# Performance work log

Hardware: AMD Instinct MI355X
Metric: run time of the kernel (lower is better)

## Reference

```python
import jax, jax.numpy as jnp
import numpy as np

HID = 2048          # hidden_size
INTER = 4096        # expand * hidden_size
NH = 64             # num_heads
HD = 64             # head_dim (NH*HD == INTER)
N = 128             # ssm state_size
G = 1               # n_groups
K = 4               # conv_kernel
EPS = 1e-5
CONV_DIM = INTER + 2 * G * N            # 4352
PROJ = INTER + CONV_DIM + NH            # 8512 (d_mlp == 0)


def setup_inputs() -> dict:
    key = jax.random.key(0)
    ks = jax.random.split(key, 6)
    B, S = 2, 2048
    return {
        "hidden_states": jax.random.normal(ks[0], (B, S, HID), jnp.float32),
        "in_proj_w": jax.random.normal(ks[1], (PROJ, HID), jnp.float32) * 0.02,
        "conv_w": jax.random.normal(ks[2], (CONV_DIM, 1, K), jnp.float32) * 0.1,
        "conv_b": jax.random.normal(ks[3], (CONV_DIM,), jnp.float32) * 0.02,
        "dt_bias": jnp.ones((NH,), jnp.float32),
        "A_log": jnp.log(jnp.arange(1, NH + 1, dtype=jnp.float32)),
        "D": jnp.ones((NH,), jnp.float32),
        "norm_weight": jnp.ones((INTER,), jnp.float32),
        "out_proj_w": jax.random.normal(ks[4], (HID, INTER), jnp.float32) * 0.02,
    }


def _mamba2_forward(hidden_states, in_proj_w, conv_w, conv_b, dt_bias,
                    A_log, D, norm_weight, out_proj_w):
    b, sq, _ = hidden_states.shape
    # in_proj (d_mlp == 0, so split is gate | hidden_B_C | dt)
    proj = hidden_states @ in_proj_w.T                       # [b, s, PROJ]
    gate, hbc, dt = jnp.split(proj, [INTER, INTER + CONV_DIM], axis=-1)

    # causal depthwise conv1d over time + SiLU
    xc = jnp.transpose(hbc, (0, 2, 1))                       # [b, conv_dim, s]
    xc = jax.lax.conv_general_dilated(xc, conv_w, (1,), [(K - 1, 0)],
                                      feature_group_count=CONV_DIM)
    xc = xc + conv_b[None, :, None]
    hbc = jax.nn.silu(jnp.transpose(xc, (0, 2, 1)))          # [b, s, conv_dim]

    hs, Bm, Cm = jnp.split(hbc, [INTER, INTER + G * N], axis=-1)
    hs = hs.reshape(b, sq, NH, HD)
    Bm = jnp.repeat(Bm.reshape(b, sq, G, N), NH // G, axis=2)   # [b, s, nh, n]
    Cm = jnp.repeat(Cm.reshape(b, sq, G, N), NH // G, axis=2)

    A = -jnp.exp(A_log)                                      # [nh]
    dt = jax.nn.softplus(dt + dt_bias)                       # [b, s, nh]

    # selective SSM scan: state_t = exp(dt*A)*state_{t-1} + dt*B_t x_t^T
    def step(state, inp):
        xt, Bt, Ct, dtt = inp                                # [b,nh,hd],[b,nh,n],[b,nh,n],[b,nh]
        dA = jnp.exp(dtt * A)                                # [b, nh]
        state = state * dA[..., None, None] \
            + (dtt[..., None] * xt)[..., None] * Bt[:, :, None, :]
        y = jnp.einsum('bhdn,bhn->bhd', state, Ct)
        return state, y

    init = jnp.zeros((b, NH, HD, N), jnp.float32)
    xs = (jnp.moveaxis(hs, 1, 0), jnp.moveaxis(Bm, 1, 0),
          jnp.moveaxis(Cm, 1, 0), jnp.moveaxis(dt, 1, 0))
    _, ys = jax.lax.scan(step, init, xs)                     # [s, b, nh, hd]
    y = jnp.moveaxis(ys, 0, 1) + D[None, None, :, None] * hs
    y = y.reshape(b, sq, INTER)

    # gated RMSNorm (norm_before_gate=False): gate first, then normalize
    y = y * jax.nn.silu(gate)
    var = jnp.mean(y * y, axis=-1, keepdims=True)
    y = y * jax.lax.rsqrt(var + EPS) * norm_weight
    return y @ out_proj_w.T                                  # [b, s, HID]


def reference(hidden_states, in_proj_w, conv_w, conv_b, dt_bias, A_log, D,
              norm_weight, out_proj_w):
    return _mamba2_forward(hidden_states, in_proj_w, conv_w, conv_b, dt_bias,
                           A_log, D, norm_weight, out_proj_w)
```

## Files before the change

kernel.cpp:

```cpp
#include <hip/hip_runtime.h>
#include <hip/hip_bf16.h>
#include <cstddef>
#include <cstdint>

#define HID   2048
#define INTER 4096
#define NH    64
#define HD    64
#define NST   128
#define CONV_DIM 4352
#define PROJ  8512
#define PROJ_PAD 8704
#define SS    2048
#define BB    2
#define BS    (BB*SS)
#define EPS   1e-5f

#define COL_HS 4096
#define COL_B  8192
#define COL_C  8320
#define COL_DT 8448

#define NCH   16
#define CHUNK 128

#define CL    128
#define NCHK  16

typedef short s16x8 __attribute__((ext_vector_type(8)));
typedef float f32x4 __attribute__((ext_vector_type(4)));

__device__ inline ushort f2b(float x) {
  __hip_bfloat16 h = __float2bfloat16(x);
  return *(ushort*)&h;
}
__device__ inline float b2f(ushort u) {
  unsigned int v = ((unsigned int)u) << 16;
  return __uint_as_float(v);
}
__device__ inline int swz(int row, int e) { return row * 128 + (e ^ ((row & 7) << 3)); }

__device__ inline void gload16(const void* g, void* l) {
  __builtin_amdgcn_global_load_lds((const __attribute__((address_space(1))) void*)g,
                                   (__attribute__((address_space(3))) void*)l, 16, 0, 0);
}

__global__ __launch_bounds__(256) void to_bf16(const float* __restrict__ src,
                                               ushort* __restrict__ dst, long n4) {
  long i = (long)blockIdx.x * 256 + threadIdx.x;
  if (i >= n4) return;
  float4 v = *(const float4*)(src + i * 4);
  ushort4 o;
  o.x = f2b(v.x); o.y = f2b(v.y); o.z = f2b(v.z); o.w = f2b(v.w);
  *(ushort4*)(dst + i * 4) = o;
}

__global__ __launch_bounds__(256) void to_bf16_pad(const float* __restrict__ src,
                                                   ushort* __restrict__ dst, long n4) {
  long i = (long)blockIdx.x * 256 + threadIdx.x;
  if (i >= n4) return;
  long e0 = i * 4;
  long row = e0 >> 11;
  ushort4 o;
  if (row < PROJ) {
    float4 v = *(const float4*)(src + e0);
    o.x = f2b(v.x); o.y = f2b(v.y); o.z = f2b(v.z); o.w = f2b(v.w);
  } else {
    o.x = o.y = o.z = o.w = 0;
  }
  *(ushort4*)(dst + e0) = o;
}

__global__ __launch_bounds__(512, 2) void gemm256_8ph(
    const ushort* __restrict__ A, const ushort* __restrict__ Bw,
    ushort* __restrict__ C, float* __restrict__ dtbuf) {
  __shared__ ushort smem[65536];
  const int tid = threadIdx.x;
  const int lane = tid & 63;
  const int wid = tid >> 6;
  const int wm = wid >> 2;
  const int wn = wid & 3;
  const int r = lane & 15;
  const int kx = lane >> 4;

  const int fid = blockIdx.x;
  const int bcol = ((fid >> 7) << 3) + ((fid & 127) >> 4);
  const int brow = fid & 15;

  const ushort* Ag = A + (size_t)(brow * 256) * HID;
  const ushort* Bg = Bw + (size_t)(bcol * 256) * HID;

  const int srow = tid >> 3;
  const int scole = (((tid & 7) * 16) ^ ((srow & 7) << 4)) >> 1;

  auto stageA = [&](int buf, int kt, int half) {
    const ushort* g = Ag + (size_t)(half * 128 + srow) * HID + kt * 64 + scole;
    ushort* l = smem + buf * 16384 + half * 8192 + tid * 8;
    gload16(g, l);
    gload16(g + (size_t)64 * HID, l + 4096);
  };
  auto stageB = [&](int buf, int kt, int half) {
    const ushort* g = Bg + (size_t)(half * 128 + srow) * HID + kt * 64 + scole;
    ushort* l = smem + 32768 + buf * 16384 + half * 8192 + tid * 8;
    gload16(g, l);
    gload16(g + (size_t)64 * HID, l + 4096);
  };
  auto ldA = [&](int buf, int mf, int ks) -> s16x8 {
    int row = wm * 128 + mf * 16 + r;
    int cb = (ks * 64 + kx * 16) ^ ((row & 7) << 4);
    return *(const s16x8*)(smem + buf * 16384 + row * 64 + (cb >> 1));
  };
  auto ldB = [&](int buf, int nf, int ks) -> s16x8 {
    int row = wn * 64 + nf * 16 + r;
    int cb = (ks * 64 + kx * 16) ^ ((row & 7) << 4);
    return *(const s16x8*)(smem + 32768 + buf * 16384 + row * 64 + (cb >> 1));
  };

  f32x4 acc[8][4];
#pragma unroll
  for (int i = 0; i < 8; i++)
#pragma unroll
    for (int j = 0; j < 4; j++) acc[i][j] = (f32x4)0.f;

  constexpr int NT = HID / 64;

  stageA(0, 0, 0); stageA(0, 0, 1);
  stageB(0, 0, 0); stageB(0, 0, 1);
  stageA(1, 1, 0); stageA(1, 1, 1);
  stageB(1, 1, 0); stageB(1, 1, 1);
  asm volatile("s_waitcnt vmcnt(8)" ::: "memory");
  __builtin_amdgcn_s_barrier();

  int cur = 0;
  for (int t = 0; t < NT; t++) {
    s16x8 a[4][2], b[2][2], b2[2][2];
#pragma unroll
    for (int mf = 0; mf < 4; mf++)
#pragma unroll
      for (int ks = 0; ks < 2; ks++) a[mf][ks] = ldA(cur, mf, ks);
#pragma unroll
    for (int nf = 0; nf < 2; nf++)
#pragma unroll
      for (int ks = 0; ks < 2; ks++) b[nf][ks] = ldB(cur, nf, ks);
    __builtin_amdgcn_s_barrier();
    asm volatile("s_waitcnt lgkmcnt(0)" ::: "memory");
    __builtin_amdgcn_sched_barrier(0);
    __builtin_amdgcn_s_setprio(1);
#pragma unroll
    for (int mf = 0; mf < 4; mf++)
#pragma unroll
      for (int nf = 0; nf < 2; nf++)
#pragma unroll
        for (int ks = 0; ks < 2; ks++)
          acc[mf][nf] = __builtin_amdgcn_mfma_f32_16x16x32_bf16(a[mf][ks], b[nf][ks], acc[mf][nf], 0, 0, 0);
    __builtin_amdgcn_s_setprio(0);
    __builtin_amdgcn_s_barrier();
#pragma unroll
    for (int nf = 0; nf < 2; nf++)
#pragma unroll
      for (int ks = 0; ks < 2; ks++) b2[nf][ks] = ldB(cur, nf + 2, ks);
    __builtin_amdgcn_s_barrier();
    asm volatile("s_waitcnt lgkmcnt(0)" ::: "memory");
    __builtin_amdgcn_sched_barrier(0);
    __builtin_amdgcn_s_setprio(1);
#pragma unroll
    for (int mf = 0; mf < 4; mf++)
#pragma unroll
      for (int nf = 0; nf < 2; nf++)
#pragma unroll
        for (int ks = 0; ks < 2; ks++)
          acc[mf][nf + 2] = __builtin_amdgcn_mfma_f32_16x16x32_bf16(a[mf][ks], b2[nf][ks], acc[mf][nf + 2], 0, 0, 0);
    __builtin_amdgcn_s_setprio(0);
    __builtin_amdgcn_s_barrier();
#pragma unroll
    for (int mf = 0; mf < 4; mf++)
#pragma unroll
      for (int ks = 0; ks < 2; ks++) a[mf][ks] = ldA(cur, mf + 4, ks);
    __builtin_amdgcn_s_barrier();
    asm volatile("s_waitcnt lgkmcnt(0)" ::: "memory");
    __builtin_amdgcn_sched_barrier(0);
    __builtin_amdgcn_s_setprio(1);
#pragma unroll
    for (int mf = 0; mf < 4; mf++)
#pragma unroll
      for (int nf = 0; nf < 2; nf++)
#pragma unroll
        for (int ks = 0; ks < 2; ks++)
          acc[mf + 4][nf] = __builtin_amdgcn_mfma_f32_16x16x32_bf16(a[mf][ks], b[nf][ks], acc[mf + 4][nf], 0, 0, 0);
    __builtin_amdgcn_s_setprio(0);
    __builtin_amdgcn_s_barrier();
    if (t + 2 < NT) {
      stageA(cur, t + 2, 0); stageA(cur, t + 2, 1);
      stageB(cur, t + 2, 0); stageB(cur, t + 2, 1);
    }
    __builtin_amdgcn_s_setprio(1);
#pragma unroll
    for (int mf = 0; mf < 4; mf++)
#pragma unroll
      for (int nf = 0; nf < 2; nf++)
#pragma unroll
        for (int ks = 0; ks < 2; ks++)
          acc[mf + 4][nf + 2] = __builtin_amdgcn_mfma_f32_16x16x32_bf16(a[mf][ks], b2[nf][ks], acc[mf + 4][nf + 2], 0, 0, 0);
    __builtin_amdgcn_s_setprio(0);
    if (t + 2 < NT) {
      asm volatile("s_waitcnt vmcnt(8)" ::: "memory");
    } else {
      asm volatile("s_waitcnt vmcnt(0)" ::: "memory");
    }
    __builtin_amdgcn_s_barrier();
    cur ^= 1;
  }

  const int m0 = brow * 256 + wm * 128 + (lane >> 4) * 4;
  const int n0 = bcol * 256 + wn * 64 + r;
#pragma unroll
  for (int mf = 0; mf < 8; mf++) {
#pragma unroll
    for (int nf = 0; nf < 4; nf++) {
      int n = n0 + nf * 16;
      if (n >= PROJ) continue;
#pragma unroll
      for (int q = 0; q < 4; q++) {
        float v = acc[mf][nf][q];
        int m = m0 + mf * 16 + q;
        C[(size_t)m * PROJ + n] = f2b(v);
        if (n >= COL_DT) dtbuf[(size_t)m * 64 + (n - COL_DT)] = v;
      }
    }
  }
}

__global__ __launch_bounds__(256) void gemm_bt16(
    const ushort* __restrict__ A, int lda,
    const ushort* __restrict__ Bw, int ldb,
    float* __restrict__ C, int ldc, int Kd) {
  __shared__ short smem[8192];
  const int tid = threadIdx.x;
  const int lane = tid & 63;
  const int wid = tid >> 6;
  const int wm = wid >> 1, wn = wid & 1;
  const int r = lane & 15;
  const int kx = lane >> 4;

  const int fid = blockIdx.y * gridDim.x + blockIdx.x;
  const int bcol = ((fid >> 8) << 3) | ((fid & 255) >> 5);
  const int brow = fid & 31;

  const ushort* Ab = A + (size_t)(brow * 128) * lda;
  const ushort* Bb = Bw + (size_t)(bcol * 128) * ldb;

  f32x4 acc[4][4];
#pragma unroll
  for (int i = 0; i < 4; i++)
#pragma unroll
    for (int j = 0; j < 4; j++) acc[i][j] = (f32x4)0.f;

  const int u0 = tid, u1 = 256 + tid;
  const int row0 = u0 >> 2, kc0 = (u0 & 3) * 8;
  const int row1 = u1 >> 2, kc1 = (u1 & 3) * 8;

  const s16x8* As8 = (const s16x8*)smem;
  const s16x8* Bs8 = (const s16x8*)(smem + 4096);

  for (int k0 = 0; k0 < Kd; k0 += 32) {
    __syncthreads();
    gload16(Ab + (size_t)row0 * lda + k0 + kc0, smem + u0 * 8);
    gload16(Ab + (size_t)row1 * lda + k0 + kc1, smem + u1 * 8);
    gload16(Bb + (size_t)row0 * ldb + k0 + kc0, smem + 4096 + u0 * 8);
    gload16(Bb + (size_t)row1 * ldb + k0 + kc1, smem + 4096 + u1 * 8);
    __syncthreads();
    s16x8 af[4], bw[4];
#pragma unroll
    for (int i = 0; i < 4; i++) af[i] = As8[(wm * 64 + i * 16 + r) * 4 + kx];
#pragma unroll
    for (int j = 0; j < 4; j++) bw[j] = Bs8[(wn * 64 + j * 16 + r) * 4 + kx];
#pragma unroll
    for (int i = 0; i < 4; i++)
#pragma unroll
      for (int j = 0; j < 4; j++)
        acc[i][j] = __builtin_amdgcn_mfma_f32_16x16x32_bf16(af[i], bw[j], acc[i][j], 0, 0, 0);
  }

  const int m0 = brow * 128 + wm * 64 + (lane >> 4) * 4;
  const int n0 = bcol * 128 + wn * 64 + (lane & 15);
#pragma unroll
  for (int i = 0; i < 4; i++) {
#pragma unroll
    for (int j = 0; j < 4; j++) {
      int n = n0 + j * 16;
#pragma unroll
      for (int q = 0; q < 4; q++) {
        C[(size_t)(m0 + i * 16 + q) * ldc + n] = acc[i][j][q];
      }
    }
  }
}

__global__ void conv_capture(const ushort* __restrict__ proj, ushort* __restrict__ side) {
  int idx = blockIdx.x * 256 + threadIdx.x;
  const int total = BB * CONV_DIM * NCH * 3;
  if (idx >= total) return;
  int c = idx % CONV_DIM;
  int t = idx / CONV_DIM;
  int j = t % 3; t /= 3;
  int chunk = t % NCH;
  int b = t / NCH;
  int s = chunk * CHUNK - 1 - j;
  ushort v = (s >= 0) ? proj[((size_t)b * SS + s) * PROJ + COL_HS + c] : (ushort)0;
  side[((size_t)(b * NCH + chunk) * 3 + j) * CONV_DIM + c] = v;
}

__global__ void conv_silu(ushort* __restrict__ proj, const ushort* __restrict__ side,
                          const float* __restrict__ cw, const float* __restrict__ cb) {
  int idx = blockIdx.x * 256 + threadIdx.x;
  const int total = BB * CONV_DIM * NCH;
  if (idx >= total) return;
  int c = idx % CONV_DIM;
  int t = idx / CONV_DIM;
  int chunk = t % NCH;
  int b = t / NCH;
  float w0 = cw[c * 4 + 0], w1 = cw[c * 4 + 1], w2 = cw[c * 4 + 2], w3 = cw[c * 4 + 3];
  float bias = cb[c];
  const ushort* sd = side + ((size_t)(b * NCH + chunk) * 3) * CONV_DIM;
  float xm1 = b2f(sd[c]);
  float xm2 = b2f(sd[CONV_DIM + c]);
  float xm3 = b2f(sd[2 * CONV_DIM + c]);
  size_t p = ((size_t)b * SS + (size_t)chunk * CHUNK) * PROJ + COL_HS + c;
  for (int s = 0; s < CHUNK; s++) {
    float xin = b2f(proj[p]);
    float o = w3 * xin + w2 * xm1 + w1 * xm2 + w0 * xm3 + bias;
    o = o / (1.f + __expf(-o));
    proj[p] = f2b(o);
    xm3 = xm2; xm2 = xm1; xm1 = xin;
    p += PROJ;
  }
}

__global__ __launch_bounds__(256) void ssd_chunk_state(
    const ushort* __restrict__ proj, const float* __restrict__ dtf,
    const float* __restrict__ dt_bias, const float* __restrict__ A_log,
    ushort* __restrict__ states, float* __restrict__ cumbuf,
    float* __restrict__ dtvbuf) {
  const int bid = blockIdx.x;
  const int c = bid & 15;
  const int h = (bid >> 4) & 63;
  const int b = bid >> 10;
  const int tid = threadIdx.x;
  const int lane = tid & 63;
  const int wv = tid >> 6;
  __shared__ float sdtv[CL], scum[CL], sw[CL];
  __shared__ ushort sBt[128 * 128];
  __shared__ ushort sXw[64 * 128];
  const size_t row0 = (size_t)b * SS + (size_t)c * CL;
  const size_t bh = (size_t)(b * NH + h);

  const float Ah = -__expf(A_log[h]);
  if (tid < CL) {
    float z = dtf[(row0 + tid) * 64 + h] + dt_bias[h];
    float dtv = (z > 20.f) ? z : log1pf(__expf(z));
    sdtv[tid] = dtv;
    sw[tid] = dtv * Ah;
  }
  __syncthreads();
  for (int off = 1; off < CL; off <<= 1) {
    float v = 0.f;
    if (tid < CL) { v = sw[tid]; if (tid >= off) v += sw[tid - off]; }
    __syncthreads();
    if (tid < CL) sw[tid] = v;
    __syncthreads();
  }
  if (tid < CL) {
    scum[tid] = sw[tid];
    cumbuf[bh * SS + c * CL + tid] = sw[tid];
    dtvbuf[bh * SS + c * CL + tid] = sdtv[tid];
  }
  __syncthreads();
  const float cumL = scum[CL - 1];
  if (tid < CL) sw[tid] = __expf(cumL - scum[tid]) * sdtv[tid];
  __syncthreads();

  {
    const int t = tid >> 1, n0 = (tid & 1) * 64;
    const ushort* src = proj + (row0 + t) * PROJ + COL_B + n0;
#pragma unroll
    for (int j = 0; j < 64; j += 8) {
      s16x8 v = *(const s16x8*)(src + j);
#pragma unroll
      for (int e = 0; e < 8; e++) sBt[swz(n0 + j + e, t)] = (ushort)v[e];
    }
  }
  {
    const int d = tid & 63;
    const int t0 = (tid >> 6) * 32;
    for (int t = t0; t < t0 + 32; t++) {
      float x = b2f(proj[(row0 + t) * PROJ + COL_HS + h * 64 + d]);
      sXw[swz(d, t)] = f2b(x * sw[t]);
    }
  }
  __syncthreads();

  const int r = lane & 15, kx = lane >> 4;
  f32x4 acc[2][4];
#pragma unroll
  for (int i = 0; i < 2; i++)
#pragma unroll
    for (int j = 0; j < 4; j++) acc[i][j] = (f32x4)0.f;
#pragma unroll
  for (int kk = 0; kk < 4; kk++) {
    s16x8 a[2], bo[4];
#pragma unroll
    for (int i = 0; i < 2; i++)
      a[i] = *(const s16x8*)&sBt[swz(wv * 32 + i * 16 + r, kk * 32 + kx * 8)];
#pragma unroll
    for (int j = 0; j < 4; j++)
      bo[j] = *(const s16x8*)&sXw[swz(j * 16 + r, kk * 32 + kx * 8)];
#pragma unroll
    for (int i = 0; i < 2; i++)
#pragma unroll
      for (int j = 0; j < 4; j++)
        acc[i][j] = __builtin_amdgcn_mfma_f32_16x16x32_bf16(a[i], bo[j], acc[i][j], 0, 0, 0);
  }
  ushort* dst = states + (size_t)bid * (128 * 64);
#pragma unroll
  for (int i = 0; i < 2; i++) {
#pragma unroll
    for (int j = 0; j < 4; j++) {
      int n = wv * 32 + i * 16 + (lane >> 4) * 4;
      int d = (lane & 15) + j * 16;
      ushort4 o;
      o.x = f2b(acc[i][j][0]);
      o.y = f2b(acc[i][j][1]);
      o.z = f2b(acc[i][j][2]);
      o.w = f2b(acc[i][j][3]);
      *(ushort4*)(dst + (size_t)d * 128 + n) = o;
    }
  }
}

__global__ __launch_bounds__(256) void ssd_state_scan(
    ushort* __restrict__ states, const float* __restrict__ cumbuf) {
  const int bh = blockIdx.x;
  const int tid = threadIdx.x;
  float run[32];
#pragma unroll
  for (int i = 0; i < 32; i++) run[i] = 0.f;
  for (int c = 0; c < NCHK; c++) {
    float dec = __expf(cumbuf[(size_t)bh * SS + c * CL + (CL - 1)]);
    ushort* p = states + ((size_t)bh * NCHK + c) * 8192 + tid * 32;
    s16x8 in[4];
#pragma unroll
    for (int v = 0; v < 4; v++) in[v] = *(const s16x8*)(p + v * 8);
    s16x8 out[4];
#pragma unroll
    for (int v = 0; v < 4; v++) {
#pragma unroll
      for (int e = 0; e < 8; e++) {
        int i = v * 8 + e;
        out[v][e] = (short)f2b(run[i]);
        run[i] = dec * run[i] + b2f((ushort)in[v][e]);
      }
    }
#pragma unroll
    for (int v = 0; v < 4; v++) *(s16x8*)(p + v * 8) = out[v];
  }
}

__global__ __launch_bounds__(256, 2) void ssd_chunk_out(
    ushort* __restrict__ proj, const ushort* __restrict__ states,
    const float* __restrict__ cumbuf, const float* __restrict__ dtvbuf,
    const float* __restrict__ Dp) {
  const int bid = blockIdx.x;
  const int c = bid & 15;
  const int h = (bid >> 4) & 63;
  const int b = bid >> 10;
  const int tid = threadIdx.x;
  const int lane = tid & 63;
  const int wv = tid >> 6;
  __shared__ ushort sC[128 * 128];
  __shared__ ushort sB[128 * 128];
  __shared__ ushort sX[64 * 128];
  const size_t row0 = (size_t)b * SS + (size_t)c * CL;
  const size_t bh = (size_t)(b * NH + h);
  const float* cumb = cumbuf + bh * SS + c * CL;
  const float* dtvb = dtvbuf + bh * SS + c * CL;
  const int r = lane & 15, kx = lane >> 4;

  float ct[2][4];
#pragma unroll
  for (int i = 0; i < 2; i++)
#pragma unroll
    for (int q = 0; q < 4; q++)
      ct[i][q] = cumb[wv * 32 + i * 16 + ((lane >> 4) << 2) + q];
  float cumt[8], dvt[8];
#pragma unroll
  for (int j = 0; j < 8; j++) {
    int tau = j * 16 + (lane & 15);
    cumt[j] = cumb[tau];
    dvt[j] = dtvb[tau];
  }
  const float eC = __expf(cumb[wv * 32 + (lane >> 1)]);

  {
    const int t = tid >> 1, n0 = (tid & 1) * 64;
    const ushort* srcC = proj + (row0 + t) * PROJ + COL_C + n0;
    const ushort* srcB = proj + (row0 + t) * PROJ + COL_B + n0;
#pragma unroll
    for (int j = 0; j < 64; j += 8) {
      *(s16x8*)&sC[swz(t, n0 + j)] = *(const s16x8*)(srcC + j);
      *(s16x8*)&sB[swz(t, n0 + j)] = *(const s16x8*)(srcB + j);
    }
  }
  {
    const int d = tid & 63;
    const int t0 = (tid >> 6) * 32;
    for (int t = t0; t < t0 + 32; t++)
      sX[swz(d, t)] = proj[(row0 + t) * PROJ + COL_HS + h * 64 + d];
  }
  __syncthreads();

  f32x4 g[2][8];
#pragma unroll
  for (int i = 0; i < 2; i++)
#pragma unroll
    for (int j = 0; j < 8; j++) g[i][j] = (f32x4)0.f;
#pragma unroll
  for (int kk = 0; kk < 4; kk++) {
    s16x8 a[2], bo[8];
#pragma unroll
    for (int i = 0; i < 2; i++)
      a[i] = *(const s16x8*)&sC[swz(wv * 32 + i * 16 + r, kk * 32 + kx * 8)];
#pragma unroll
    for (int j = 0; j < 8; j++)
      bo[j] = *(const s16x8*)&sB[swz(j * 16 + r, kk * 32 + kx * 8)];
#pragma unroll
    for (int i = 0; i < 2; i++)
#pragma unroll
      for (int j = 0; j < 8; j++)
        g[i][j] = __builtin_amdgcn_mfma_f32_16x16x32_bf16(a[i], bo[j], g[i][j], 0, 0, 0);
  }

  s16x8 spf[4][4];
  {
    const ushort* sp = states + (size_t)bid * 8192;
#pragma unroll
    for (int kk = 0; kk < 4; kk++)
#pragma unroll
      for (int j = 0; j < 4; j++)
        spf[kk][j] = *(const s16x8*)(sp + (size_t)(j * 16 + r) * 128 + kk * 32 + kx * 8);
  }
  __syncthreads();

#pragma unroll
  for (int j = 0; j < 8; j++) {
    float cu = cumt[j], dv = dvt[j];
    int tau = j * 16 + (lane & 15);
#pragma unroll
    for (int i = 0; i < 2; i++) {
#pragma unroll
      for (int q = 0; q < 4; q++) {
        int t = wv * 32 + i * 16 + ((lane >> 4) << 2) + q;
        float val = (tau <= t) ? g[i][j][q] * __expf(ct[i][q] - cu) * dv : 0.f;
        sB[swz(t, tau)] = f2b(val);
      }
    }
  }
  {
    int t = wv * 32 + (lane >> 1);
    int n0 = (lane & 1) * 64;
#pragma unroll
    for (int j = 0; j < 64; j += 8) {
      s16x8 u = *(const s16x8*)&sC[swz(t, n0 + j)];
#pragma unroll
      for (int k = 0; k < 8; k++) u[k] = (short)f2b(b2f((ushort)u[k]) * eC);
      *(s16x8*)&sC[swz(t, n0 + j)] = u;
    }
  }
  __syncthreads();

  f32x4 y[2][4];
#pragma unroll
  for (int i = 0; i < 2; i++)
#pragma unroll
    for (int j = 0; j < 4; j++) y[i][j] = (f32x4)0.f;
#pragma unroll
  for (int kk = 0; kk < 4; kk++) {
    s16x8 a[2], bo[4];
#pragma unroll
    for (int i = 0; i < 2; i++)
      a[i] = *(const s16x8*)&sB[swz(wv * 32 + i * 16 + r, kk * 32 + kx * 8)];
#pragma unroll
    for (int j = 0; j < 4; j++)
      bo[j] = *(const s16x8*)&sX[swz(j * 16 + r, kk * 32 + kx * 8)];
#pragma unroll
    for (int i = 0; i < 2; i++)
#pragma unroll
      for (int j = 0; j < 4; j++)
        y[i][j] = __builtin_amdgcn_mfma_f32_16x16x32_bf16(a[i], bo[j], y[i][j], 0, 0, 0);
  }
#pragma unroll
  for (int kk = 0; kk < 4; kk++) {
    s16x8 a[2];
#pragma unroll
    for (int i = 0; i < 2; i++)
      a[i] = *(const s16x8*)&sC[swz(wv * 32 + i * 16 + r, kk * 32 + kx * 8)];
#pragma unroll
    for (int i = 0; i < 2; i++)
#pragma unroll
      for (int j = 0; j < 4; j++)
        y[i][j] = __builtin_amdgcn_mfma_f32_16x16x32_bf16(a[i], spf[kk][j], y[i][j], 0, 0, 0);
  }

  const float Dh = Dp[h];
#pragma unroll
  for (int i = 0; i < 2; i++) {
#pragma unroll
    for (int j = 0; j < 4; j++) {
      int t0 = wv * 32 + i * 16 + (lane >> 4) * 4;
      int d = (lane & 15) + j * 16;
#pragma unroll
      for (int q = 0; q < 4; q++) {
        float x = b2f(sX[swz(d, t0 + q)]);
        proj[(row0 + t0 + q) * PROJ + COL_HS + h * 64 + d] = f2b(y[i][j][q] + Dh * x);
      }
    }
  }
}

__global__ __launch_bounds__(256) void rmsnorm_kernel(
    ushort* __restrict__ proj, const float* __restrict__ nw) {
  const int row = blockIdx.x;
  const int tid = threadIdx.x;
  ushort* yp = proj + (size_t)row * PROJ + COL_HS;
  const ushort* gp = proj + (size_t)row * PROJ;
  float v[16];
  float ss = 0.f;
#pragma unroll
  for (int q = 0; q < 4; q++) {
    int col = q * 1024 + tid * 4;
    ushort4 yv = *(const ushort4*)(yp + col);
    ushort4 gv = *(const ushort4*)(gp + col);
    float vy[4] = {b2f(yv.x), b2f(yv.y), b2f(yv.z), b2f(yv.w)};
    float vg[4] = {b2f(gv.x), b2f(gv.y), b2f(gv.z), b2f(gv.w)};
#pragma unroll
    for (int j = 0; j < 4; j++) {
      float sg = vg[j] / (1.f + __expf(-vg[j]));
      float vv = vy[j] * sg;
      v[q * 4 + j] = vv;
      ss += vv * vv;
    }
  }
#pragma unroll
  for (int o = 1; o < 64; o <<= 1) ss += __shfl_xor(ss, o);
  __shared__ float red[4];
  if ((tid & 63) == 0) red[tid >> 6] = ss;
  __syncthreads();
  float tot = red[0] + red[1] + red[2] + red[3];
  float scale = rsqrtf(tot * (1.f / INTER) + EPS);
#pragma unroll
  for (int q = 0; q < 4; q++) {
    int col = q * 1024 + tid * 4;
    float4 w = *(const float4*)(nw + col);
    ushort4 o;
    o.x = f2b(v[q * 4 + 0] * scale * w.x);
    o.y = f2b(v[q * 4 + 1] * scale * w.y);
    o.z = f2b(v[q * 4 + 2] * scale * w.z);
    o.w = f2b(v[q * 4 + 3] * scale * w.w);
    *(ushort4*)(yp + col) = o;
  }
}

extern "C" void kernel_launch(void* const* d_in, const int* in_sizes, int n_in,
                              void* d_out, int out_size, void* d_ws, size_t ws_size,
                              hipStream_t stream) {
  const float* hs   = (const float*)d_in[0];
  const float* w1   = (const float*)d_in[1];
  const float* cw   = (const float*)d_in[2];
  const float* cb   = (const float*)d_in[3];
  const float* dtb  = (const float*)d_in[4];
  const float* alog = (const float*)d_in[5];
  const float* Dp   = (const float*)d_in[6];
  const float* nw   = (const float*)d_in[7];
  const float* w2   = (const float*)d_in[8];
  float* out = (float*)d_out;

  char* base = (char*)d_ws;
  size_t off = 0;
  ushort* proj = (ushort*)(base + off); off += (size_t)BS * PROJ * 2;
  ushort* side = (ushort*)(base + off); off += (size_t)BB * NCH * 3 * CONV_DIM * 2;
  off = (off + 255) & ~(size_t)255;
  float* dtbuf = (float*)(base + off); off += (size_t)BS * 64 * 4;
  off = (off + 255) & ~(size_t)255;
  char* rC = base + off;
  ushort* hs16 = (ushort*)rC;
  ushort* w1p  = (ushort*)(rC + 16777216);
  ushort* states = (ushort*)rC;
  float*  cumbuf = (float*)(rC + 33554432);
  float*  dtvbuf = (float*)(rC + 33554432 + 1048576);
  ushort* w216 = (ushort*)rC;

  {
    long n4 = (long)BS * HID / 4;
    to_bf16<<<(n4 + 255) / 256, 256, 0, stream>>>(hs, hs16, n4);
  }
  {
    long n4 = (long)PROJ_PAD * HID / 4;
    to_bf16_pad<<<(n4 + 255) / 256, 256, 0, stream>>>(w1, w1p, n4);
  }

  gemm256_8ph<<<(BS / 256) * (PROJ_PAD / 256), 512, 0, stream>>>(hs16, w1p, proj, dtbuf);

  conv_capture<<<(BB * CONV_DIM * NCH * 3 + 255) / 256, 256, 0, stream>>>(proj, side);
  conv_silu<<<(BB * CONV_DIM * NCH + 255) / 256, 256, 0, stream>>>(proj, side, cw, cb);

  ssd_chunk_state<<<BB * NH * NCHK, 256, 0, stream>>>(proj, dtbuf, dtb, alog, states, cumbuf, dtvbuf);
  ssd_state_scan<<<BB * NH, 256, 0, stream>>>(states, cumbuf);
  ssd_chunk_out<<<BB * NH * NCHK, 256, 0, stream>>>(proj, states, cumbuf, dtvbuf, Dp);

  {
    long n4 = (long)HID * INTER / 4;
    to_bf16<<<(n4 + 255) / 256, 256, 0, stream>>>(w2, w216, n4);
  }

  rmsnorm_kernel<<<BS, 256, 0, stream>>>(proj, nw);

  gemm_bt16<<<dim3(HID / 128, BS / 128), 256, 0, stream>>>(
      (const ushort*)(proj + COL_HS), PROJ, w216, INTER, out, HID, INTER);
}
```

Before: 478.0 us.

## Pipeline out_proj GEMM with 256x128 swizzled double-buffered tiles; restage B loads in in_proj

Replaces the simple single-buffered 128x128 out_proj GEMM with a 512-thread 256x128 kernel. It stages 64-wide K tiles into XOR-swizzled LDS double buffers using async global-to-LDS loads, waits on vmcnt, and gives the MFMA phases raised priority. This is meant to hide global load latency and cut the per-K-step syncthreads stalls. It also changes the in_proj GEMM so B tiles for the next step are staged one iteration ahead, interleaved between the LDS read phases, rather than two steps ahead alongside A. That spreads memory traffic across the loop, but it relies on the buffer-reuse timing and the adjusted vmcnt counts being correct.

```diff
diff --git a/kernel.cpp b/kernel.cpp
--- a/kernel.cpp
+++ b/kernel.cpp
@@ -127,8 +127,7 @@
   stageA(0, 0, 0); stageA(0, 0, 1);
   stageB(0, 0, 0); stageB(0, 0, 1);
   stageA(1, 1, 0); stageA(1, 1, 1);
-  stageB(1, 1, 0); stageB(1, 1, 1);
-  asm volatile("s_waitcnt vmcnt(8)" ::: "memory");
+  asm volatile("s_waitcnt vmcnt(4)" ::: "memory");
   __builtin_amdgcn_s_barrier();
 
   int cur = 0;
@@ -142,6 +141,7 @@
     for (int nf = 0; nf < 2; nf++)
 #pragma unroll
       for (int ks = 0; ks < 2; ks++) b[nf][ks] = ldB(cur, nf, ks);
+    if (t + 1 < NT) stageB(cur ^ 1, t + 1, 0);
     __builtin_amdgcn_s_barrier();
     asm volatile("s_waitcnt lgkmcnt(0)" ::: "memory");
     __builtin_amdgcn_sched_barrier(0);
@@ -159,6 +159,7 @@
     for (int nf = 0; nf < 2; nf++)
 #pragma unroll
       for (int ks = 0; ks < 2; ks++) b2[nf][ks] = ldB(cur, nf + 2, ks);
+    if (t + 1 < NT) stageB(cur ^ 1, t + 1, 1);
     __builtin_amdgcn_s_barrier();
     asm volatile("s_waitcnt lgkmcnt(0)" ::: "memory");
     __builtin_amdgcn_sched_barrier(0);
@@ -189,10 +190,7 @@
           acc[mf + 4][nf] = __builtin_amdgcn_mfma_f32_16x16x32_bf16(a[mf][ks], b[nf][ks], acc[mf + 4][nf], 0, 0, 0);
     __builtin_amdgcn_s_setprio(0);
     __builtin_amdgcn_s_barrier();
-    if (t + 2 < NT) {
-      stageA(cur, t + 2, 0); stageA(cur, t + 2, 1);
-      stageB(cur, t + 2, 0); stageB(cur, t + 2, 1);
-    }
+    if (t + 2 < NT) { stageA(cur, t + 2, 0); stageA(cur, t + 2, 1); }
     __builtin_amdgcn_s_setprio(1);
 #pragma unroll
     for (int mf = 0; mf < 4; mf++)
@@ -203,7 +201,7 @@
           acc[mf + 4][nf + 2] = __builtin_amdgcn_mfma_f32_16x16x32_bf16(a[mf][ks], b2[nf][ks], acc[mf + 4][nf + 2], 0, 0, 0);
     __builtin_amdgcn_s_setprio(0);
     if (t + 2 < NT) {
-      asm volatile("s_waitcnt vmcnt(8)" ::: "memory");
+      asm volatile("s_waitcnt vmcnt(4)" ::: "memory");
     } else {
       asm volatile("s_waitcnt vmcnt(0)" ::: "memory");
     }
@@ -230,24 +228,52 @@
   }
 }
 
-__global__ __launch_bounds__(256) void gemm_bt16(
-    const ushort* __restrict__ A, int lda,
-    const ushort* __restrict__ Bw, int ldb,
-    float* __restrict__ C, int ldc, int Kd) {
-  __shared__ short smem[8192];
+__global__ __launch_bounds__(512, 2) void gemm2_256x128(
+    const ushort* __restrict__ A, const ushort* __restrict__ Bw,
+    float* __restrict__ C) {
+  __shared__ ushort smem[49152];
   const int tid = threadIdx.x;
   const int lane = tid & 63;
   const int wid = tid >> 6;
-  const int wm = wid >> 1, wn = wid & 1;
+  const int wm = wid >> 1;
+  const int wn = wid & 1;
   const int r = lane & 15;
   const int kx = lane >> 4;
 
-  const int fid = blockIdx.y * gridDim.x + blockIdx.x;
-  const int bcol = ((fid >> 8) << 3) | ((fid & 255) >> 5);
-  const int brow = fid & 31;
-
-  const ushort* Ab = A + (size_t)(brow * 128) * lda;
-  const ushort* Bb = Bw + (size_t)(bcol * 128) * ldb;
+  const int fid = blockIdx.x;
+  const int bcol = fid >> 4;
+  const int brow = fid & 15;
+
+  const ushort* Ag = A + (size_t)(brow * 256) * PROJ;
+  const ushort* Bg = Bw + (size_t)(bcol * 128) * INTER;
+
+  const int srow = tid >> 3;
+  const int scole = (((tid & 7) * 16) ^ ((srow & 7) << 4)) >> 1;
+
+  auto stageA2 = [&](int buf, int kt) {
+#pragma unroll
+    for (int i = 0; i < 4; i++) {
+      gload16(Ag + (size_t)(i * 64 + srow) * PROJ + kt * 64 + scole,
+              smem + buf * 16384 + i * 4096 + tid * 8);
+    }
+  };
+  auto stageB2 = [&](int buf, int kt) {
+#pragma unroll
+    for (int i = 0; i < 2; i++) {
+      gload16(Bg + (size_t)(i * 64 + srow) * INTER + kt * 64 + scole,
+              smem + 32768 + buf * 8192 + i * 4096 + tid * 8);
+    }
+  };
+  auto ldA2 = [&](int buf, int mf, int ks) -> s16x8 {
+    int row = wm * 64 + mf * 16 + r;
+    int cb = (ks * 64 + kx * 16) ^ ((row & 7) << 4);
+    return *(const s16x8*)(smem + buf * 16384 + row * 64 + (cb >> 1));
+  };
+  auto ldB2 = [&](int buf, int nf, int ks) -> s16x8 {
+    int row = wn * 64 + nf * 16 + r;
+    int cb = (ks * 64 + kx * 16) ^ ((row & 7) << 4);
+    return *(const s16x8*)(smem + 32768 + buf * 8192 + row * 64 + (cb >> 1));
+  };
 
   f32x4 acc[4][4];
 #pragma unroll
@@ -255,43 +281,66 @@
 #pragma unroll
     for (int j = 0; j < 4; j++) acc[i][j] = (f32x4)0.f;
 
-  const int u0 = tid, u1 = 256 + tid;
-  const int row0 = u0 >> 2, kc0 = (u0 & 3) * 8;
-  const int row1 = u1 >> 2, kc1 = (u1 & 3) * 8;
-
-  const s16x8* As8 = (const s16x8*)smem;
-  const s16x8* Bs8 = (const s16x8*)(smem + 4096);
-
-  for (int k0 = 0; k0 < Kd; k0 += 32) {
-    __syncthreads();
-    gload16(Ab + (size_t)row0 * lda + k0 + kc0, smem + u0 * 8);
-    gload16(Ab + (size_t)row1 * lda + k0 + kc1, smem + u1 * 8);
-    gload16(Bb + (size_t)row0 * ldb + k0 + kc0, smem + 4096 + u0 * 8);
-    gload16(Bb + (size_t)row1 * ldb + k0 + kc1, smem + 4096 + u1 * 8);
-    __syncthreads();
-    s16x8 af[4], bw[4];
-#pragma unroll
-    for (int i = 0; i < 4; i++) af[i] = As8[(wm * 64 + i * 16 + r) * 4 + kx];
-#pragma unroll
-    for (int j = 0; j < 4; j++) bw[j] = Bs8[(wn * 64 + j * 16 + r) * 4 + kx];
-#pragma unroll
-    for (int i = 0; i < 4; i++)
-#pragma unroll
-      for (int j = 0; j < 4; j++)
-        acc[i][j] = __builtin_amdgcn_mfma_f32_16x16x32_bf16(af[i], bw[j], acc[i][j], 0, 0, 0);
-  }
-
-  const int m0 = brow * 128 + wm * 64 + (lane >> 4) * 4;
-  const int n0 = bcol * 128 + wn * 64 + (lane & 15);
-#pragma unroll
-  for (int i = 0; i < 4; i++) {
-#pragma unroll
-    for (int j = 0; j < 4; j++) {
-      int n = n0 + j * 16;
-#pragma unroll
-      for (int q = 0; q < 4; q++) {
-        C[(size_t)(m0 + i * 16 + q) * ldc + n] = acc[i][j][q];
-      }
+  constexpr int NT = INTER / 64;
+
+  stageA2(0, 0); stageB2(0, 0);
+  stageA2(1, 1); stageB2(1, 1);
+  asm volatile("s_waitcnt vmcnt(6)" ::: "memory");
+  __builtin_amdgcn_s_barrier();
+
+  int cur = 0;
+  for (int t = 0; t < NT; t++) {
+    s16x8 a[4][2], b[4][2];
+#pragma unroll
+    for (int mf = 0; mf < 4; mf++)
+#pragma unroll
+      for (int ks = 0; ks < 2; ks++) a[mf][ks] = ldA2(cur, mf, ks);
+#pragma unroll
+    for (int nf = 0; nf < 4; nf++)
+#pragma unroll
+      for (int ks = 0; ks < 2; ks++) b[nf][ks] = ldB2(cur, nf, ks);
+    __builtin_amdgcn_s_barrier();
+    asm volatile("s_waitcnt lgkmcnt(0)" ::: "memory");
+    __builtin_amdgcn_sched_barrier(0);
+    __builtin_amdgcn_s_setprio(1);
+#pragma unroll
+    for (int mf = 0; mf < 4; mf++)
+#pragma unroll
+      for (int nf = 0; nf < 2; nf++)
+#pragma unroll
+        for (int ks = 0; ks < 2; ks++)
+          acc[mf][nf] = __builtin_amdgcn_mfma_f32_16x16x32_bf16(a[mf][ks], b[nf][ks], acc[mf][nf], 0, 0, 0);
+    __builtin_amdgcn_s_setprio(0);
+    __builtin_amdgcn_s_barrier();
+    if (t + 2 < NT) { stageA2(cur, t + 2); stageB2(cur, t + 2); }
+    __builtin_amdgcn_s_setprio(1);
+#pragma unroll
+    for (int mf = 0; mf < 4; mf++)
+#pragma unroll
+      for (int nf = 2; nf < 4; nf++)
+#pragma unroll
+        for (int ks = 0; ks < 2; ks++)
+          acc[mf][nf] = __builtin_amdgcn_mfma_f32_16x16x32_bf16(a[mf][ks], b[nf][ks], acc[mf][nf], 0, 0, 0);
+    __builtin_amdgcn_s_setprio(0);
+    if (t + 2 < NT) {
+      asm volatile("s_waitcnt vmcnt(6)" ::: "memory");
+    } else {
+      asm volatile("s_waitcnt vmcnt(0)" ::: "memory");
+    }
+    __builtin_amdgcn_s_barrier();
+    cur ^= 1;
+  }
+
+  const int m0 = brow * 256 + wm * 64 + (lane >> 4) * 4;
+  const int n0 = bcol * 128 + wn * 64 + r;
+#pragma unroll
+  for (int mf = 0; mf < 4; mf++) {
+#pragma unroll
+    for (int nf = 0; nf < 4; nf++) {
+      int n = n0 + nf * 16;
+#pragma unroll
+      for (int q = 0; q < 4; q++)
+        C[(size_t)(m0 + mf * 16 + q) * HID + n] = acc[mf][nf][q];
     }
   }
 }
@@ -723,6 +772,6 @@
 
   rmsnorm_kernel<<<BS, 256, 0, stream>>>(proj, nw);
 
-  gemm_bt16<<<dim3(HID / 128, BS / 128), 256, 0, stream>>>(
-      (const ushort*)(proj + COL_HS), PROJ, w216, INTER, out, HID, INTER);
-}
+  gemm2_256x128<<<256, 512, 0, stream>>>(
+      (const ushort*)(proj + COL_HS), w216, out);
+}
```

New measurement: 441.4 us. -7.7%, faster.
